# Performance work log

Measured on AMD Instinct MI355X. Metric: run time of the kernel, lower is better.

## Reference

```python
import jax, jax.numpy as jnp
import numpy as np
from jax.scipy.special import gammaln

EPS = 1e-20
EULER_GAMMA = 0.5772156649015329
B, L, D, H, DK, DV = 8, 512, 1024, 16, 64, 64
K_WEIBULL = 0.5
BETA_GAMMA = 1.0
SCALE = 1.0 / np.sqrt(DK)  # torch code DIVIDES by this -> multiply by sqrt(DK)


def setup_inputs() -> dict:
    key = jax.random.key(0)
    ks = jax.random.split(key, 20)
    f = jnp.float32
    return {
        "queries": jax.random.normal(ks[0], (B, L, D), f),
        "keys": jax.random.normal(ks[1], (B, L, D), f),
        "values": jax.random.normal(ks[2], (B, L, D), f),
        "unif": jax.random.uniform(ks[3], (B, H, L, L), f),
        "Wq": jax.random.normal(ks[4], (D, H * DK), f) * 0.03,
        "bq": jnp.zeros((H * DK,), f),
        "Wk": jax.random.normal(ks[5], (D, H * DK), f) * 0.03,
        "bk": jnp.zeros((H * DK,), f),
        "Wv": jax.random.normal(ks[6], (D, H * DV), f) * 0.03,
        "bv": jnp.zeros((H * DV,), f),
        "Wo": jax.random.normal(ks[7], (H * DV, D), f) * 0.03,
        "bo": jnp.zeros((D,), f),
        "Wp1": jax.random.normal(ks[8], (DK, D), f) * 0.05,
        "bp1": jnp.zeros((D,), f),
        "Wp2": jax.random.normal(ks[9], (D, 1), f) * 0.05,
        "bp2": jnp.zeros((1,), f),
    }


def reference(queries, keys, values, unif, Wq, bq, Wk, bk, Wv, bv, Wo, bo, Wp1, bp1, Wp2, bp2):
    # projections -> multi-head layout
    q = (queries @ Wq + bq).reshape(B, L, H, DK).transpose(0, 2, 1, 3)   # [B,H,Q,dk]
    k = (keys @ Wk + bk).reshape(B, L, H, DK).transpose(0, 2, 1, 3)     # [B,H,K,dk]
    v = (values @ Wv + bv).reshape(B, L, H, DV).transpose(0, 2, 1, 3)   # [B,H,K,dv]

    # faithful: torch divides by scale=1/sqrt(dk)
    att = jnp.einsum("bhqd,bhkd->bhqk", q, k) / SCALE                   # [B,H,Q,K]

    # prior MLP on keys (per key position)
    h = (k @ Wp1 + bp1)                                                  # [B,H,K,D]
    h = jnp.where(h >= 0, h, 0.01 * h)                                   # LeakyReLU
    dot_gamma = (h @ Wp2 + bp2).transpose(0, 1, 3, 2)                    # [B,H,1,K]
    prior_w = jax.nn.softmax(dot_gamma, axis=-1)
    alpha = prior_w * BETA_GAMMA                                         # [B,H,1,K]

    # Weibull reparameterized stochastic attention
    inv_k = 1.0 / K_WEIBULL
    logprobs = jnp.log(jax.nn.softmax(att, axis=-1) + EPS)
    gumbel_w = jnp.log(-jnp.log(1.0 - unif + EPS) + EPS)
    att_s = jax.nn.softmax(logprobs - gammaln(1.0 + inv_k + inv_k * gumbel_w), axis=-1)

    lg1 = gammaln(jnp.float32(1.0 + inv_k))
    kl = -(alpha * (logprobs - lg1)
           - EULER_GAMMA * alpha * inv_k
           - BETA_GAMMA * jnp.exp(logprobs - lg1 + lg1)
           + alpha * jnp.log(BETA_GAMMA + EPS)
           - gammaln(alpha + EPS))
    kl_mean = kl.mean()

    out = jnp.einsum("bhqk,bhkd->bhqd", att_s, v)                        # [B,H,Q,dv]
    out = out.transpose(0, 2, 1, 3).reshape(B, L, H * DV)
    out = out @ Wo + bo                                                  # [B,Q,D]
    return out, kl_mean
```

## Files before the change

### kernel.cpp

```cpp
#include <hip/hip_runtime.h>
#include <math.h>


typedef __bf16 bh_t;
typedef bh_t  bh8  __attribute__((ext_vector_type(8)));
typedef float f32x4 __attribute__((ext_vector_type(4)));
typedef _Float16 hf_t;
typedef hf_t  hf4  __attribute__((ext_vector_type(4)));

#define MFMA_BF16 __builtin_amdgcn_mfma_f32_16x16x32_bf16

static constexpr size_t P2 = 4096ull*1024ull*2ull;
static constexpr size_t W2 = 1024ull*1024ull*2ull;
static constexpr size_t O_QHI = 0;
static constexpr size_t O_QLO = O_QHI + P2;
static constexpr size_t O_KHI = O_QLO + P2;
static constexpr size_t O_KLO = O_KHI + P2;
static constexpr size_t O_VT  = O_KLO + P2;
static constexpr size_t O_WQH = O_VT  + P2;
static constexpr size_t O_WQL = O_WQH + W2;
static constexpr size_t O_WKH = O_WQL + W2;
static constexpr size_t O_WKL = O_WKH + W2;
static constexpr size_t O_WVH = O_WKL + W2;
static constexpr size_t O_WVL = O_WVH + W2;
static constexpr size_t O_WOH = O_WVL + W2;
static constexpr size_t O_WOL = O_WOH + W2;
static constexpr size_t O_WP1H = O_WOL + W2;
static constexpr size_t O_WP1L = O_WP1H + 1024ull*64ull*2ull;
static constexpr size_t O_DG   = O_WP1L + 1024ull*64ull*2ull;
static constexpr size_t O_ALPHA= O_DG + 65536ull*4ull;
static constexpr size_t O_HO   = O_ALPHA + 65536ull*4ull;
static constexpr size_t O_GS   = O_HO + P2;
static constexpr size_t O_ACC  = O_GS + 512ull*65536ull*2ull;
static constexpr size_t WS_TOTAL = O_ACC + 256;

__device__ __align__(256) unsigned char g_ws[WS_TOTAL];

__device__ __forceinline__ float lgamma_fast(float x)
{
    float ax = (x < 0.5f) ? (1.0f - x) : x;
    float p  = ax*(ax+1.f)*(ax+2.f)*(ax+3.f);
    bool  sm = ax < 4.0f;
    float lsh = sm ? __logf(p) : 0.0f;
    float y   = sm ? (ax + 4.0f) : ax;
    float ly  = __logf(y);
    float inv = __builtin_amdgcn_rcpf(y);
    float i2  = inv * inv;
    float stir = fmaf(y - 0.5f, ly, -y) + 0.91893853320467274f
               + inv * fmaf(-2.7777777777e-3f, i2, 8.3333333333e-2f);
    float core = stir - lsh;
    float r  = x - rintf(x);
    float sp = __sinf(3.14159265358979f * r);
    float rres = 1.14472988584940017f - __logf(fabsf(sp)) - core;
    return (x < 0.5f) ? rres : core;
}

__global__ void k_zero(double* a)
{
    if (threadIdx.x < 4) a[threadIdx.x] = 0.0;
}

__global__ __launch_bounds__(256) void k_transpose_split(
    const float* __restrict__ in, bh_t* __restrict__ oh, bh_t* __restrict__ ol,
    int rows, int cols)
{
    __shared__ float tile[64][65];
    const int bc = blockIdx.x * 64, br = blockIdx.y * 64;
    const int t = threadIdx.x;
    const int r = t >> 2, c0 = (t & 3) * 16;
#pragma unroll
    for (int i = 0; i < 16; i += 4) {
        float4 v = *(const float4*)(in + (size_t)(br + r) * cols + bc + c0 + i);
        tile[r][c0+i]   = v.x; tile[r][c0+i+1] = v.y;
        tile[r][c0+i+2] = v.z; tile[r][c0+i+3] = v.w;
    }
    __syncthreads();
    bh8 hv[2], lv[2];
#pragma unroll
    for (int i = 0; i < 16; i++) {
        float x = tile[c0 + i][r];
        bh_t hh = (bh_t)x;
        hv[i >> 3][i & 7] = hh;
        lv[i >> 3][i & 7] = (bh_t)(x - (float)hh);
    }
    size_t ob = (size_t)(bc + r) * rows + br + c0;
    *(bh8*)(oh + ob)     = hv[0];
    *(bh8*)(oh + ob + 8) = hv[1];
    *(bh8*)(ol + ob)     = lv[0];
    *(bh8*)(ol + ob + 8) = lv[1];
}

__global__ __launch_bounds__(256) void k_transpose_split4(
    const float* __restrict__ W0, const float* __restrict__ W1,
    const float* __restrict__ W2_, const float* __restrict__ W3,
    bh_t* __restrict__ OH)
{
    __shared__ float tile[64][65];
    const int z = blockIdx.z;
    const float* in = (z == 0) ? W0 : (z == 1) ? W1 : (z == 2) ? W2_ : W3;
    bh_t* oh = OH + (size_t)z * 2ull * 1024ull * 1024ull;
    bh_t* ol = oh + 1024ull * 1024ull;
    const int bc = blockIdx.x * 64, br = blockIdx.y * 64;
    const int t = threadIdx.x;
    const int r = t >> 2, c0 = (t & 3) * 16;
#pragma unroll
    for (int i = 0; i < 16; i += 4) {
        float4 v = *(const float4*)(in + (size_t)(br + r) * 1024 + bc + c0 + i);
        tile[r][c0+i]   = v.x; tile[r][c0+i+1] = v.y;
        tile[r][c0+i+2] = v.z; tile[r][c0+i+3] = v.w;
    }
    __syncthreads();
    bh8 hv[2], lv[2];
#pragma unroll
    for (int i = 0; i < 16; i++) {
        float x = tile[c0 + i][r];
        bh_t hh = (bh_t)x;
        hv[i >> 3][i & 7] = hh;
        lv[i >> 3][i & 7] = (bh_t)(x - (float)hh);
    }
    size_t ob = (size_t)(bc + r) * 1024 + br + c0;
    *(bh8*)(oh + ob)     = hv[0];
    *(bh8*)(oh + ob + 8) = hv[1];
    *(bh8*)(ol + ob)     = lv[0];
    *(bh8*)(ol + ob + 8) = lv[1];
}

template<bool SPLIT, int OMODE, bool ABF>
__device__ __forceinline__ void gemm_body(
    const float* __restrict__ A, const bh_t* __restrict__ ABH,
    const bh_t* __restrict__ WH, const bh_t* __restrict__ WL,
    const float* __restrict__ bias,
    bh_t* __restrict__ oh, bh_t* __restrict__ ol, float* __restrict__ of,
    int n0, int m0)
{
    __shared__ __align__(16) bh_t Ah[128][40];
    __shared__ __align__(16) bh_t Al[128][40];
    __shared__ __align__(16) bh_t Bh[64][40];
    __shared__ __align__(16) bh_t Bl[64][40];
    const int t = threadIdx.x;
    const int lane = t & 63, w = t >> 6;
    const int lr = lane & 15, kg = lane >> 4;
    const int wm = (w & 1) * 64, wn = (w >> 1) * 32;
    const int ar = t >> 2, ac = (t & 3) * 8;
    f32x4 acc[4][2] = {};

    for (int kt = 0; kt < 1024; kt += 32) {
        __syncthreads();
        {
            if constexpr (ABF) {
                *(bh8*)&Ah[ar][ac]      = *(const bh8*)(ABH + (size_t)(m0 + ar) * 1024 + kt + ac);
                *(bh8*)&Ah[ar + 64][ac] = *(const bh8*)(ABH + (size_t)(m0 + ar + 64) * 1024 + kt + ac);
            } else {
#pragma unroll
                for (int half = 0; half < 2; half++) {
                    const float* ap = A + (size_t)(m0 + ar + half*64) * 1024 + kt + ac;
                    float4 v0 = *(const float4*)ap;
                    float4 v1 = *(const float4*)(ap + 4);
                    float xs[8] = {v0.x, v0.y, v0.z, v0.w, v1.x, v1.y, v1.z, v1.w};
                    bh8 h, l;
#pragma unroll
                    for (int i = 0; i < 8; i++) {
                        bh_t hh = (bh_t)xs[i];
                        h[i] = hh;
                        l[i] = (bh_t)(xs[i] - (float)hh);
                    }
                    *(bh8*)&Ah[ar + half*64][ac] = h;
                    if constexpr (SPLIT) *(bh8*)&Al[ar + half*64][ac] = l;
                }
            }
            size_t wb = (size_t)(n0 + ar) * 1024 + kt + ac;
            *(bh8*)&Bh[ar][ac] = *(const bh8*)(WH + wb);
            if constexpr (SPLIT) *(bh8*)&Bl[ar][ac] = *(const bh8*)(WL + wb);
        }
        __syncthreads();
#pragma unroll
        for (int fm = 0; fm < 4; fm++) {
            bh8 a_h = *(bh8*)&Ah[wm + fm*16 + lr][kg * 8];
            bh8 a_l;
            if constexpr (SPLIT) a_l = *(bh8*)&Al[wm + fm*16 + lr][kg * 8];
#pragma unroll
            for (int fn = 0; fn < 2; fn++) {
                bh8 b_h = *(bh8*)&Bh[wn + fn*16 + lr][kg * 8];
                acc[fm][fn] = MFMA_BF16(a_h, b_h, acc[fm][fn], 0, 0, 0);
                if constexpr (SPLIT) {
                    bh8 b_l = *(bh8*)&Bl[wn + fn*16 + lr][kg * 8];
                    acc[fm][fn] = MFMA_BF16(a_h, b_l, acc[fm][fn], 0, 0, 0);
                    acc[fm][fn] = MFMA_BF16(a_l, b_h, acc[fm][fn], 0, 0, 0);
                }
            }
        }
    }
#pragma unroll
    for (int fm = 0; fm < 4; fm++)
#pragma unroll
    for (int fn = 0; fn < 2; fn++) {
        int col = n0 + wn + fn*16 + lr;
        float bv = bias[col];
#pragma unroll
        for (int r = 0; r < 4; r++) {
            int row = m0 + wm + fm*16 + kg*4 + r;
            float c = acc[fm][fn][r] + bv;
            size_t idx = (size_t)row * 1024 + col;
            if constexpr (OMODE == 0) {
                bh_t hh = (bh_t)c;
                oh[idx] = hh;
                ol[idx] = (bh_t)(c - (float)hh);
            } else if constexpr (OMODE == 1) {
                oh[idx] = (bh_t)c;
            } else if constexpr (OMODE == 2) {
                of[idx] = c;
            } else {
                int bb = row >> 9, ll = row & 511;
                oh[(((size_t)(bb*16 + (col >> 6)) * 64) + (col & 63)) * 512 + ll] = (bh_t)c;
            }
        }
    }
}

template<bool SPLIT, int OMODE, bool ABF>
__global__ __launch_bounds__(256) void k_gemm(
    const float* __restrict__ A, const bh_t* __restrict__ ABH,
    const bh_t* __restrict__ WH, const bh_t* __restrict__ WL,
    const float* __restrict__ bias,
    bh_t* __restrict__ oh, bh_t* __restrict__ ol, float* __restrict__ of)
{
    gemm_body<SPLIT, OMODE, ABF>(A, ABH, WH, WL, bias, oh, ol, of,
                                 blockIdx.x * 64, blockIdx.y * 128);
}

__global__ __launch_bounds__(256) void k_gemm_qk(
    const float* __restrict__ Aq, const float* __restrict__ Ak,
    const bh_t* __restrict__ Wbase, const float* __restrict__ bq,
    const float* __restrict__ bk, bh_t* __restrict__ Obase)
{
    const int z = blockIdx.z;
    const float* A = z ? Ak : Aq;
    const bh_t* WH = Wbase + (size_t)z * 2ull * 1024ull * 1024ull;
    const bh_t* WL = WH + 1024ull * 1024ull;
    const float* bias = z ? bk : bq;
    bh_t* oh = Obase + (size_t)z * 2ull * 4096ull * 1024ull;
    bh_t* ol = oh + 4096ull * 1024ull;
    gemm_body<true, 0, false>(A, nullptr, WH, WL, bias, oh, ol, nullptr,
                              blockIdx.x * 64, blockIdx.y * 128);
}

__global__ __launch_bounds__(256) void k_prior(
    const bh_t* __restrict__ KH, const bh_t* __restrict__ WP1T,
    const float* __restrict__ bp1, const float* __restrict__ wp2,
    const float* __restrict__ bp2, float* __restrict__ DG)
{
    __shared__ __align__(16) bh_t Kt[64][72];
    __shared__ __align__(16) bh_t Wt[64][72];
    const int lt = blockIdx.x, h = blockIdx.y, b = blockIdx.z;
    const int t = threadIdx.x, lane = t & 63, w = t >> 6;
    const int lr = lane & 15, kg = lane >> 4;
    {
        int r = t >> 2, j0 = (t & 3) * 16;
        const bh_t* src = KH + ((size_t)(b*512 + lt*64 + r)) * 1024 + h*64 + j0;
        *(bh8*)&Kt[r][j0]     = *(const bh8*)src;
        *(bh8*)&Kt[r][j0 + 8] = *(const bh8*)(src + 8);
    }
    __syncthreads();
    bh8 af0 = *(bh8*)&Kt[w*16 + lr][kg * 8];
    bh8 af1 = *(bh8*)&Kt[w*16 + lr][32 + kg * 8];
    float dgp[4] = {0.f, 0.f, 0.f, 0.f};
    for (int dt = 0; dt < 16; dt++) {
        __syncthreads();
        {
            int r = t >> 2, j0 = (t & 3) * 16;
            const bh_t* src = WP1T + (size_t)(dt*64 + r) * 64 + j0;
            *(bh8*)&Wt[r][j0]     = *(const bh8*)src;
            *(bh8*)&Wt[r][j0 + 8] = *(const bh8*)(src + 8);
        }
        __syncthreads();
#pragma unroll
        for (int fn = 0; fn < 4; fn++) {
            bh8 b0 = *(bh8*)&Wt[fn*16 + lr][kg * 8];
            bh8 b1 = *(bh8*)&Wt[fn*16 + lr][32 + kg * 8];
            f32x4 acc = {};
            acc = MFMA_BF16(af0, b0, acc, 0, 0, 0);
            acc = MFMA_BF16(af1, b1, acc, 0, 0, 0);
            int d = dt*64 + fn*16 + lr;
            float bpv = bp1[d], wvv = wp2[d];
#pragma unroll
            for (int r = 0; r < 4; r++) {
                float hv = acc[r] + bpv;
                hv = (hv >= 0.f) ? hv : 0.01f * hv;
                dgp[r] = fmaf(hv, wvv, dgp[r]);
            }
        }
    }
#pragma unroll
    for (int r = 0; r < 4; r++) {
        float v = dgp[r];
        v += __shfl_xor(v, 1); v += __shfl_xor(v, 2);
        v += __shfl_xor(v, 4); v += __shfl_xor(v, 8);
        dgp[r] = v;
    }
    if (lr == 0) {
        float b2 = bp2[0];
        int bh = b * 16 + h;
#pragma unroll
        for (int r = 0; r < 4; r++)
            DG[(size_t)bh*512 + lt*64 + w*16 + kg*4 + r] = dgp[r] + b2;
    }
}

__global__ __launch_bounds__(512) void k_alpha(
    const float* __restrict__ DG, float* __restrict__ AL, double* __restrict__ acc)
{
    __shared__ float red[512];
    const int bh = blockIdx.x, t = threadIdx.x;
    float v = DG[(size_t)bh * 512 + t];
    red[t] = v; __syncthreads();
    for (int s = 256; s > 0; s >>= 1) { if (t < s) red[t] = fmaxf(red[t], red[t+s]); __syncthreads(); }
    float m = red[0]; __syncthreads();
    float e = expf(v - m);
    red[t] = e; __syncthreads();
    for (int s = 256; s > 0; s >>= 1) { if (t < s) red[t] += red[t+s]; __syncthreads(); }
    float ssum = red[0]; __syncthreads();
    float a = e / ssum;
    AL[(size_t)bh * 512 + t] = a;
    float t2 = a * 1.8475785103630112f + lgammaf(a + 1e-20f);
    red[t] = t2; __syncthreads();
    for (int s = 256; s > 0; s >>= 1) { if (t < s) red[t] += red[t+s]; __syncthreads(); }
    if (t == 0) atomicAdd(&acc[2], (double)red[0]);
}

__global__ __launch_bounds__(512, 3) void k_attn(
    const bh_t* __restrict__ QH, const bh_t* __restrict__ QL,
    const bh_t* __restrict__ KH, const bh_t* __restrict__ KL,
    const bh_t* __restrict__ VT, const float* __restrict__ U,
    const float* __restrict__ AL, bh_t* __restrict__ HOB,
    hf_t* __restrict__ GS, double* __restrict__ acc)
{
    __shared__ __align__(16) bh_t KtH[64][72];
    __shared__ __align__(16) bh_t KtL[64][72];
    __shared__ __align__(16) bh_t Vt[64][72];
    __shared__ __align__(16) bh_t Sl[8][16][72];
    __shared__ float Asm[64];
    __shared__ float red[512];

    const int flat = blockIdx.x;
    const int bh = flat & 127, qc = flat >> 7;
    const int b = bh >> 4, h = bh & 15;
    const int t = threadIdx.x, w = t >> 6, lane = t & 63;
    const int lr = lane & 15, kg = lane >> 4;
    const int q0 = qc * 128 + w * 16;
    const int sr = t >> 3, sj = (t & 7) * 8;
    const float* Up = U + ((size_t)bh * 512 + q0 + kg * 4) * 512;
    hf_t* GSp = GS + (size_t)flat * 65536 + (size_t)w * 8192;

    bh8 qh[2], ql[2];
    {
        size_t qb = ((size_t)(b * 512) + q0 + lr) * 1024 + h * 64;
        qh[0] = *(const bh8*)(QH + qb + kg * 8);
        qh[1] = *(const bh8*)(QH + qb + 32 + kg * 8);
        ql[0] = *(const bh8*)(QL + qb + kg * 8);
        ql[1] = *(const bh8*)(QL + qb + 32 + kg * 8);
    }
    float C[4];

    {
        float M1[4], Z1[4];
#pragma unroll
        for (int r = 0; r < 4; r++) { M1[r] = -INFINITY; Z1[r] = 0.f; }

        for (int kt = 0; kt < 8; kt++) {
            __syncthreads();
            {
                size_t src = ((size_t)(b*512 + kt*64 + sr)) * 1024 + h*64 + sj;
                *(bh8*)&KtH[sr][sj] = *(const bh8*)(KH + src);
                *(bh8*)&KtL[sr][sj] = *(const bh8*)(KL + src);
            }
            __syncthreads();
            f32x4 av[4];
#pragma unroll
            for (int fn = 0; fn < 4; fn++) {
                f32x4 a = {};
#pragma unroll
                for (int ks = 0; ks < 2; ks++) {
                    bh8 kb  = *(bh8*)&KtH[fn*16 + lr][ks*32 + kg*8];
                    bh8 kl2 = *(bh8*)&KtL[fn*16 + lr][ks*32 + kg*8];
                    a = MFMA_BF16(qh[ks], kb,  a, 0, 0, 0);
                    a = MFMA_BF16(qh[ks], kl2, a, 0, 0, 0);
                    a = MFMA_BF16(ql[ks], kb,  a, 0, 0, 0);
                }
#pragma unroll
                for (int r = 0; r < 4; r++) a[r] *= 8.0f;
                av[fn] = a;
                int k = kt * 64 + fn * 16 + lr;
                hf4 gh;
#pragma unroll
                for (int r = 0; r < 4; r++) {
                    float u  = Up[(size_t)r * 512 + k];
                    float tt = (1.0f - u) + 1e-20f;
                    float gl = 1e-20f - __logf(tt);
                    float g  = __logf(gl);
                    gh[r] = (hf_t)lgamma_fast(fmaf(2.0f, g, 3.0f));
                }
                *(hf4*)(GSp + ((size_t)(kt*4 + fn) * 64 + lane) * 4) = gh;
            }
#pragma unroll
            for (int r = 0; r < 4; r++) {
                float mx = fmaxf(fmaxf(av[0][r], av[1][r]), fmaxf(av[2][r], av[3][r]));
                mx = fmaxf(mx, __shfl_xor(mx, 1));
                mx = fmaxf(mx, __shfl_xor(mx, 2));
                mx = fmaxf(mx, __shfl_xor(mx, 4));
                mx = fmaxf(mx, __shfl_xor(mx, 8));
                float nm = fmaxf(M1[r], mx);
                float es = __expf(av[0][r]-nm) + __expf(av[1][r]-nm)
                         + __expf(av[2][r]-nm) + __expf(av[3][r]-nm);
                es += __shfl_xor(es, 1); es += __shfl_xor(es, 2);
                es += __shfl_xor(es, 4); es += __shfl_xor(es, 8);
                Z1[r] = Z1[r] * __expf(M1[r] - nm) + es;
                M1[r] = nm;
            }
        }
#pragma unroll
        for (int r = 0; r < 4; r++) C[r] = M1[r] + logf(Z1[r]);
    }

    float M2[4], Z2[4];
    f32x4 oacc[4] = {};
#pragma unroll
    for (int r = 0; r < 4; r++) { M2[r] = -INFINITY; Z2[r] = 0.f; }
    float S1f = 0.f;

    for (int kt = 0; kt < 8; kt++) {
        __syncthreads();
        {
            size_t src = ((size_t)(b*512 + kt*64 + sr)) * 1024 + h*64 + sj;
            *(bh8*)&KtH[sr][sj] = *(const bh8*)(KH + src);
            *(bh8*)&KtL[sr][sj] = *(const bh8*)(KL + src);
            const bh_t* vsrc = VT + ((size_t)bh * 64 + sr) * 512 + kt*64 + sj;
            *(bh8*)&Vt[sr][sj] = *(const bh8*)vsrc;
            if (t < 64) Asm[t] = AL[(size_t)bh * 512 + kt * 64 + t];
        }
        __syncthreads();
        f32x4 wv[4];
#pragma unroll
        for (int fn = 0; fn < 4; fn++) {
            f32x4 a = {};
#pragma unroll
            for (int ks = 0; ks < 2; ks++) {
                bh8 kb  = *(bh8*)&KtH[fn*16 + lr][ks*32 + kg*8];
                bh8 kl2 = *(bh8*)&KtL[fn*16 + lr][ks*32 + kg*8];
                a = MFMA_BF16(qh[ks], kb,  a, 0, 0, 0);
                a = MFMA_BF16(qh[ks], kl2, a, 0, 0, 0);
                a = MFMA_BF16(ql[ks], kb,  a, 0, 0, 0);
            }
            hf4 gh = *(const hf4*)(GSp + ((size_t)(kt*4 + fn) * 64 + lane) * 4);
            float alv = Asm[fn * 16 + lr];
#pragma unroll
            for (int r = 0; r < 4; r++) {
                float s  = fmaf(a[r], 8.0f, -C[r]);
                float ex = __expf(s);
                float lp = __logf(ex + 1e-20f);
                wv[fn][r] = lp - (float)gh[r];
                S1f = fmaf(alv, lp, S1f);
            }
        }
#pragma unroll
        for (int r = 0; r < 4; r++) {
            float mx = fmaxf(fmaxf(wv[0][r], wv[1][r]), fmaxf(wv[2][r], wv[3][r]));
            mx = fmaxf(mx, __shfl_xor(mx, 1));
            mx = fmaxf(mx, __shfl_xor(mx, 2));
            mx = fmaxf(mx, __shfl_xor(mx, 4));
            mx = fmaxf(mx, __shfl_xor(mx, 8));
            float nm = fmaxf(M2[r], mx);
            float sc = __expf(M2[r] - nm);
            float zs = 0.f;
#pragma unroll
            for (int fn = 0; fn < 4; fn++) {
                float sv = __expf(wv[fn][r] - nm);
                zs += sv;
                Sl[w][kg * 4 + r][fn * 16 + lr] = (bh_t)sv;
            }
            zs += __shfl_xor(zs, 1); zs += __shfl_xor(zs, 2);
            zs += __shfl_xor(zs, 4); zs += __shfl_xor(zs, 8);
            Z2[r] = fmaf(Z2[r], sc, zs);
            M2[r] = nm;
#pragma unroll
            for (int fo = 0; fo < 4; fo++) oacc[fo][r] *= sc;
        }
        bh8 sa0 = *(bh8*)&Sl[w][lr][kg*8];
        bh8 sa1 = *(bh8*)&Sl[w][lr][32 + kg*8];
#pragma unroll
        for (int fo = 0; fo < 4; fo++) {
            bh8 v0 = *(bh8*)&Vt[fo*16 + lr][kg*8];
            bh8 v1 = *(bh8*)&Vt[fo*16 + lr][32 + kg*8];
            oacc[fo] = MFMA_BF16(sa0, v0, oacc[fo], 0, 0, 0);
            oacc[fo] = MFMA_BF16(sa1, v1, oacc[fo], 0, 0, 0);
        }
    }
    float rz[4];
#pragma unroll
    for (int r = 0; r < 4; r++) rz[r] = 1.0f / Z2[r];
#pragma unroll
    for (int fo = 0; fo < 4; fo++) {
#pragma unroll
        for (int r = 0; r < 4; r++) {
            int q = q0 + kg * 4 + r;
            int dv = fo * 16 + lr;
            HOB[((size_t)(b * 512 + q)) * 1024 + h * 64 + dv] = (bh_t)(oacc[fo][r] * rz[r]);
        }
    }
    red[t] = S1f; __syncthreads();
    for (int s = 256; s > 0; s >>= 1) { if (t < s) red[t] += red[t+s]; __syncthreads(); }
    if (t == 0) atomicAdd(&acc[0], (double)red[0]);
}

__global__ void k_kl(const double* __restrict__ acc, float* __restrict__ out)
{
    if (threadIdx.x == 0 && blockIdx.x == 0) {
        double kl = (-acc[0] + 512.0 * acc[2] + 65536.0) / 33554432.0;
        out[4194304] = (float)kl;
    }
}

extern "C" void kernel_launch(void* const* d_in, const int* in_sizes, int n_in,
                              void* d_out, int out_size, void* d_ws, size_t ws_size,
                              hipStream_t stream)
{
    (void)in_sizes; (void)n_in; (void)d_ws; (void)ws_size; (void)out_size;
    const float* queries = (const float*)d_in[0];
    const float* keys    = (const float*)d_in[1];
    const float* values  = (const float*)d_in[2];
    const float* unif    = (const float*)d_in[3];
    const float* Wq = (const float*)d_in[4];  const float* bq = (const float*)d_in[5];
    const float* Wk = (const float*)d_in[6];  const float* bk = (const float*)d_in[7];
    const float* Wv = (const float*)d_in[8];  const float* bv = (const float*)d_in[9];
    const float* Wo = (const float*)d_in[10]; const float* bo = (const float*)d_in[11];
    const float* Wp1 = (const float*)d_in[12]; const float* bp1 = (const float*)d_in[13];
    const float* Wp2 = (const float*)d_in[14]; const float* bp2 = (const float*)d_in[15];

    unsigned char* ws = nullptr;
    hipGetSymbolAddress((void**)&ws, HIP_SYMBOL(g_ws));

    bh_t* QHI = (bh_t*)(ws + O_QHI);
    bh_t* KHI = (bh_t*)(ws + O_KHI); bh_t* KLO = (bh_t*)(ws + O_KLO);
    bh_t* QLO = (bh_t*)(ws + O_QLO);
    bh_t* VTp = (bh_t*)(ws + O_VT);
    bh_t* WQH = (bh_t*)(ws + O_WQH);
    bh_t* WVH = (bh_t*)(ws + O_WVH); bh_t* WVL = (bh_t*)(ws + O_WVL);
    bh_t* WOH = (bh_t*)(ws + O_WOH); bh_t* WOL = (bh_t*)(ws + O_WOL);
    bh_t* WP1H = (bh_t*)(ws + O_WP1H); bh_t* WP1L = (bh_t*)(ws + O_WP1L);
    float* DG    = (float*)(ws + O_DG);
    float* ALPHA = (float*)(ws + O_ALPHA);
    bh_t*  HOB   = (bh_t*)(ws + O_HO);
    hf_t*  GS    = (hf_t*)(ws + O_GS);
    double* ACC  = (double*)(ws + O_ACC);
    float* outF  = (float*)d_out;

    k_zero<<<1, 64, 0, stream>>>(ACC);

    k_transpose_split4<<<dim3(16,16,4), 256, 0, stream>>>(Wq, Wk, Wv, Wo, WQH);
    k_transpose_split<<<dim3(16,1), 256, 0, stream>>>(Wp1, WP1H, WP1L, 64, 1024);

    k_gemm_qk<<<dim3(16,32,2), 256, 0, stream>>>(queries, keys, WQH, bq, bk, QHI);
    k_gemm<false,3,false><<<dim3(16,32), 256, 0, stream>>>(values, nullptr, WVH, WVL, bv, VTp, nullptr, nullptr);

    k_prior<<<dim3(8,16,8), 256, 0, stream>>>(KHI, WP1H, bp1, Wp2, bp2, DG);
    k_alpha<<<128, 512, 0, stream>>>(DG, ALPHA, ACC);

    k_attn<<<512, 512, 0, stream>>>(QHI, QLO, KHI, KLO, VTp, unif, ALPHA, HOB, GS, ACC);

    k_gemm<false,2,true><<<dim3(16,32), 256, 0, stream>>>(nullptr, HOB, WOH, WOL, bo, nullptr, nullptr, outF);
    k_kl<<<1, 1, 0, stream>>>(ACC, outF);
}
```

Baseline: 358.8 us.

## Pre-split activations to bf16, enlarge GEMM tile to 128x128, fuse tiny kernels

Adds a separate kernel that converts the query, key and value activations to bf16 hi/lo pairs once, so the GEMM blocks no longer repeat the fp32 conversion on every tile load. The GEMM tile grows from 128x64 to 128x128 with B fragments hoisted into registers, which gives more MFMA reuse per loaded element and halves the number of blocks. The accumulator zeroing and the final KL write are folded into existing kernels, removing two launches. In exchange it adds extra workspace traffic for the split activations, uses more registers and LDS per block, and launches fewer blocks, which may underfill the GPU.

```diff
diff --git a/kernel.cpp b/kernel.cpp
--- a/kernel.cpp
+++ b/kernel.cpp
@@ -10,7 +10,8 @@
 
 #define MFMA_BF16 __builtin_amdgcn_mfma_f32_16x16x32_bf16
 
-static constexpr size_t P2 = 4096ull*1024ull*2ull;
+static constexpr size_t PE = 4096ull*1024ull;
+static constexpr size_t P2 = PE*2ull;
 static constexpr size_t W2 = 1024ull*1024ull*2ull;
 static constexpr size_t O_QHI = 0;
 static constexpr size_t O_QLO = O_QHI + P2;
@@ -32,7 +33,8 @@
 static constexpr size_t O_HO   = O_ALPHA + 65536ull*4ull;
 static constexpr size_t O_GS   = O_HO + P2;
 static constexpr size_t O_ACC  = O_GS + 512ull*65536ull*2ull;
-static constexpr size_t WS_TOTAL = O_ACC + 256;
+static constexpr size_t O_AQH  = O_ACC + 256;
+static constexpr size_t WS_TOTAL = O_AQH + 5ull*P2;
 
 __device__ __align__(256) unsigned char g_ws[WS_TOTAL];
 
@@ -55,11 +57,6 @@
     return (x < 0.5f) ? rres : core;
 }
 
-__global__ void k_zero(double* a)
-{
-    if (threadIdx.x < 4) a[threadIdx.x] = 0.0;
-}
-
 __global__ __launch_bounds__(256) void k_transpose_split(
     const float* __restrict__ in, bh_t* __restrict__ oh, bh_t* __restrict__ ol,
     int rows, int cols)
@@ -93,10 +90,12 @@
 __global__ __launch_bounds__(256) void k_transpose_split4(
     const float* __restrict__ W0, const float* __restrict__ W1,
     const float* __restrict__ W2_, const float* __restrict__ W3,
-    bh_t* __restrict__ OH)
+    bh_t* __restrict__ OH, double* __restrict__ acc)
 {
     __shared__ float tile[64][65];
     const int z = blockIdx.z;
+    if (z == 0 && blockIdx.x == 0 && blockIdx.y == 0 && threadIdx.x < 4)
+        acc[threadIdx.x] = 0.0;
     const float* in = (z == 0) ? W0 : (z == 1) ? W1 : (z == 2) ? W2_ : W3;
     bh_t* oh = OH + (size_t)z * 2ull * 1024ull * 1024ull;
     bh_t* ol = oh + 1024ull * 1024ull;
@@ -125,9 +124,35 @@
     *(bh8*)(ol + ob + 8) = lv[1];
 }
 
-template<bool SPLIT, int OMODE, bool ABF>
+__global__ __launch_bounds__(256) void k_splitA(
+    const float* __restrict__ q, const float* __restrict__ k,
+    const float* __restrict__ v, bh_t* __restrict__ dst)
+{
+    const int z = blockIdx.y;
+    const float* in = (z == 0) ? q : (z == 1) ? k : v;
+    size_t idx = ((size_t)blockIdx.x * 256 + threadIdx.x) * 8;
+    float4 v0 = *(const float4*)(in + idx);
+    float4 v1 = *(const float4*)(in + idx + 4);
+    float xs[8] = {v0.x, v0.y, v0.z, v0.w, v1.x, v1.y, v1.z, v1.w};
+    bh8 h, l;
+#pragma unroll
+    for (int i = 0; i < 8; i++) {
+        bh_t hh = (bh_t)xs[i];
+        h[i] = hh;
+        l[i] = (bh_t)(xs[i] - (float)hh);
+    }
+    if (z < 2) {
+        bh_t* hp = dst + (size_t)z * 2 * PE;
+        *(bh8*)(hp + idx)      = h;
+        *(bh8*)(hp + PE + idx) = l;
+    } else {
+        *(bh8*)(dst + 4 * PE + idx) = h;
+    }
+}
+
+template<bool SPLIT, int OMODE>
 __device__ __forceinline__ void gemm_body(
-    const float* __restrict__ A, const bh_t* __restrict__ ABH,
+    const bh_t* __restrict__ ABH, const bh_t* __restrict__ ABL,
     const bh_t* __restrict__ WH, const bh_t* __restrict__ WL,
     const float* __restrict__ bias,
     bh_t* __restrict__ oh, bh_t* __restrict__ ol, float* __restrict__ of,
@@ -135,57 +160,53 @@
 {
     __shared__ __align__(16) bh_t Ah[128][40];
     __shared__ __align__(16) bh_t Al[128][40];
-    __shared__ __align__(16) bh_t Bh[64][40];
-    __shared__ __align__(16) bh_t Bl[64][40];
+    __shared__ __align__(16) bh_t Bh[128][40];
+    __shared__ __align__(16) bh_t Bl[128][40];
     const int t = threadIdx.x;
     const int lane = t & 63, w = t >> 6;
     const int lr = lane & 15, kg = lane >> 4;
-    const int wm = (w & 1) * 64, wn = (w >> 1) * 32;
+    const int wm = (w & 1) * 64, wn = (w >> 1) * 64;
     const int ar = t >> 2, ac = (t & 3) * 8;
-    f32x4 acc[4][2] = {};
+    f32x4 acc[4][4] = {};
 
     for (int kt = 0; kt < 1024; kt += 32) {
         __syncthreads();
         {
-            if constexpr (ABF) {
-                *(bh8*)&Ah[ar][ac]      = *(const bh8*)(ABH + (size_t)(m0 + ar) * 1024 + kt + ac);
-                *(bh8*)&Ah[ar + 64][ac] = *(const bh8*)(ABH + (size_t)(m0 + ar + 64) * 1024 + kt + ac);
-            } else {
-#pragma unroll
-                for (int half = 0; half < 2; half++) {
-                    const float* ap = A + (size_t)(m0 + ar + half*64) * 1024 + kt + ac;
-                    float4 v0 = *(const float4*)ap;
-                    float4 v1 = *(const float4*)(ap + 4);
-                    float xs[8] = {v0.x, v0.y, v0.z, v0.w, v1.x, v1.y, v1.z, v1.w};
-                    bh8 h, l;
-#pragma unroll
-                    for (int i = 0; i < 8; i++) {
-                        bh_t hh = (bh_t)xs[i];
-                        h[i] = hh;
-                        l[i] = (bh_t)(xs[i] - (float)hh);
-                    }
-                    *(bh8*)&Ah[ar + half*64][ac] = h;
-                    if constexpr (SPLIT) *(bh8*)&Al[ar + half*64][ac] = l;
-                }
-            }
-            size_t wb = (size_t)(n0 + ar) * 1024 + kt + ac;
-            *(bh8*)&Bh[ar][ac] = *(const bh8*)(WH + wb);
-            if constexpr (SPLIT) *(bh8*)&Bl[ar][ac] = *(const bh8*)(WL + wb);
+            size_t a0 = (size_t)(m0 + ar) * 1024 + kt + ac;
+            size_t a1 = (size_t)(m0 + ar + 64) * 1024 + kt + ac;
+            *(bh8*)&Ah[ar][ac]      = *(const bh8*)(ABH + a0);
+            *(bh8*)&Ah[ar + 64][ac] = *(const bh8*)(ABH + a1);
+            if constexpr (SPLIT) {
+                *(bh8*)&Al[ar][ac]      = *(const bh8*)(ABL + a0);
+                *(bh8*)&Al[ar + 64][ac] = *(const bh8*)(ABL + a1);
+            }
+            size_t b0 = (size_t)(n0 + ar) * 1024 + kt + ac;
+            size_t b1 = (size_t)(n0 + ar + 64) * 1024 + kt + ac;
+            *(bh8*)&Bh[ar][ac]      = *(const bh8*)(WH + b0);
+            *(bh8*)&Bh[ar + 64][ac] = *(const bh8*)(WH + b1);
+            if constexpr (SPLIT) {
+                *(bh8*)&Bl[ar][ac]      = *(const bh8*)(WL + b0);
+                *(bh8*)&Bl[ar + 64][ac] = *(const bh8*)(WL + b1);
+            }
         }
         __syncthreads();
+        bh8 bfh[4], bfl[4];
+#pragma unroll
+        for (int fn = 0; fn < 4; fn++) {
+            bfh[fn] = *(bh8*)&Bh[wn + fn*16 + lr][kg * 8];
+            if constexpr (SPLIT) bfl[fn] = *(bh8*)&Bl[wn + fn*16 + lr][kg * 8];
+        }
 #pragma unroll
         for (int fm = 0; fm < 4; fm++) {
             bh8 a_h = *(bh8*)&Ah[wm + fm*16 + lr][kg * 8];
             bh8 a_l;
             if constexpr (SPLIT) a_l = *(bh8*)&Al[wm + fm*16 + lr][kg * 8];
 #pragma unroll
-            for (int fn = 0; fn < 2; fn++) {
-                bh8 b_h = *(bh8*)&Bh[wn + fn*16 + lr][kg * 8];
-                acc[fm][fn] = MFMA_BF16(a_h, b_h, acc[fm][fn], 0, 0, 0);
+            for (int fn = 0; fn < 4; fn++) {
+                acc[fm][fn] = MFMA_BF16(a_h, bfh[fn], acc[fm][fn], 0, 0, 0);
                 if constexpr (SPLIT) {
-                    bh8 b_l = *(bh8*)&Bl[wn + fn*16 + lr][kg * 8];
-                    acc[fm][fn] = MFMA_BF16(a_h, b_l, acc[fm][fn], 0, 0, 0);
-                    acc[fm][fn] = MFMA_BF16(a_l, b_h, acc[fm][fn], 0, 0, 0);
+                    acc[fm][fn] = MFMA_BF16(a_h, bfl[fn], acc[fm][fn], 0, 0, 0);
+                    acc[fm][fn] = MFMA_BF16(a_l, bfh[fn], acc[fm][fn], 0, 0, 0);
                 }
             }
         }
@@ -193,7 +214,7 @@
 #pragma unroll
     for (int fm = 0; fm < 4; fm++)
 #pragma unroll
-    for (int fn = 0; fn < 2; fn++) {
+    for (int fn = 0; fn < 4; fn++) {
         int col = n0 + wn + fn*16 + lr;
         float bv = bias[col];
 #pragma unroll
@@ -217,31 +238,36 @@
     }
 }
 
-template<bool SPLIT, int OMODE, bool ABF>
+template<int OMODE>
 __global__ __launch_bounds__(256) void k_gemm(
-    const float* __restrict__ A, const bh_t* __restrict__ ABH,
+    const bh_t* __restrict__ ABH,
     const bh_t* __restrict__ WH, const bh_t* __restrict__ WL,
     const float* __restrict__ bias,
-    bh_t* __restrict__ oh, bh_t* __restrict__ ol, float* __restrict__ of)
-{
-    gemm_body<SPLIT, OMODE, ABF>(A, ABH, WH, WL, bias, oh, ol, of,
-                                 blockIdx.x * 64, blockIdx.y * 128);
+    bh_t* __restrict__ oh, float* __restrict__ of,
+    const double* __restrict__ acc)
+{
+    gemm_body<false, OMODE>(ABH, nullptr, WH, WL, bias, oh, nullptr, of,
+                            blockIdx.x * 128, blockIdx.y * 128);
+    if constexpr (OMODE == 2) {
+        if (blockIdx.x == 0 && blockIdx.y == 0 && threadIdx.x == 0) {
+            double kl = (-acc[0] + 512.0 * acc[2] + 65536.0) / 33554432.0;
+            of[4194304] = (float)kl;
+        }
+    }
 }
 
 __global__ __launch_bounds__(256) void k_gemm_qk(
-    const float* __restrict__ Aq, const float* __restrict__ Ak,
-    const bh_t* __restrict__ Wbase, const float* __restrict__ bq,
-    const float* __restrict__ bk, bh_t* __restrict__ Obase)
+    const bh_t* __restrict__ Abase, const bh_t* __restrict__ Wbase,
+    const float* __restrict__ bq, const float* __restrict__ bk,
+    bh_t* __restrict__ Obase)
 {
     const int z = blockIdx.z;
-    const float* A = z ? Ak : Aq;
+    const bh_t* AH = Abase + (size_t)z * 2 * PE;
     const bh_t* WH = Wbase + (size_t)z * 2ull * 1024ull * 1024ull;
-    const bh_t* WL = WH + 1024ull * 1024ull;
-    const float* bias = z ? bk : bq;
-    bh_t* oh = Obase + (size_t)z * 2ull * 4096ull * 1024ull;
-    bh_t* ol = oh + 4096ull * 1024ull;
-    gemm_body<true, 0, false>(A, nullptr, WH, WL, bias, oh, ol, nullptr,
-                              blockIdx.x * 64, blockIdx.y * 128);
+    bh_t* oh = Obase + (size_t)z * 2 * PE;
+    gemm_body<true, 0>(AH, AH + PE, WH, WH + 1024ull*1024ull,
+                       z ? bk : bq, oh, oh + PE, nullptr,
+                       blockIdx.x * 128, blockIdx.y * 128);
 }
 
 __global__ __launch_bounds__(256) void k_prior(
@@ -511,14 +537,6 @@
     if (t == 0) atomicAdd(&acc[0], (double)red[0]);
 }
 
-__global__ void k_kl(const double* __restrict__ acc, float* __restrict__ out)
-{
-    if (threadIdx.x == 0 && blockIdx.x == 0) {
-        double kl = (-acc[0] + 512.0 * acc[2] + 65536.0) / 33554432.0;
-        out[4194304] = (float)kl;
-    }
-}
-
 extern "C" void kernel_launch(void* const* d_in, const int* in_sizes, int n_in,
                               void* d_out, int out_size, void* d_ws, size_t ws_size,
                               hipStream_t stream)
@@ -538,9 +556,8 @@
     unsigned char* ws = nullptr;
     hipGetSymbolAddress((void**)&ws, HIP_SYMBOL(g_ws));
 
-    bh_t* QHI = (bh_t*)(ws + O_QHI);
+    bh_t* QHI = (bh_t*)(ws + O_QHI); bh_t* QLO = (bh_t*)(ws + O_QLO);
     bh_t* KHI = (bh_t*)(ws + O_KHI); bh_t* KLO = (bh_t*)(ws + O_KLO);
-    bh_t* QLO = (bh_t*)(ws + O_QLO);
     bh_t* VTp = (bh_t*)(ws + O_VT);
     bh_t* WQH = (bh_t*)(ws + O_WQH);
     bh_t* WVH = (bh_t*)(ws + O_WVH); bh_t* WVL = (bh_t*)(ws + O_WVL);
@@ -551,21 +568,21 @@
     bh_t*  HOB   = (bh_t*)(ws + O_HO);
     hf_t*  GS    = (hf_t*)(ws + O_GS);
     double* ACC  = (double*)(ws + O_ACC);
+    bh_t*  AQH   = (bh_t*)(ws + O_AQH);
+    bh_t*  AVH   = AQH + 4 * PE;
     float* outF  = (float*)d_out;
 
-    k_zero<<<1, 64, 0, stream>>>(ACC);
-
-    k_transpose_split4<<<dim3(16,16,4), 256, 0, stream>>>(Wq, Wk, Wv, Wo, WQH);
+    k_transpose_split4<<<dim3(16,16,4), 256, 0, stream>>>(Wq, Wk, Wv, Wo, WQH, ACC);
     k_transpose_split<<<dim3(16,1), 256, 0, stream>>>(Wp1, WP1H, WP1L, 64, 1024);
-
-    k_gemm_qk<<<dim3(16,32,2), 256, 0, stream>>>(queries, keys, WQH, bq, bk, QHI);
-    k_gemm<false,3,false><<<dim3(16,32), 256, 0, stream>>>(values, nullptr, WVH, WVL, bv, VTp, nullptr, nullptr);
+    k_splitA<<<dim3(2048,3), 256, 0, stream>>>(queries, keys, values, AQH);
+
+    k_gemm_qk<<<dim3(8,32,2), 256, 0, stream>>>(AQH, WQH, bq, bk, QHI);
+    k_gemm<3><<<dim3(8,32), 256, 0, stream>>>(AVH, WVH, WVL, bv, VTp, nullptr, nullptr);
 
     k_prior<<<dim3(8,16,8), 256, 0, stream>>>(KHI, WP1H, bp1, Wp2, bp2, DG);
     k_alpha<<<128, 512, 0, stream>>>(DG, ALPHA, ACC);
 
     k_attn<<<512, 512, 0, stream>>>(QHI, QLO, KHI, KLO, VTp, unif, ALPHA, HOB, GS, ACC);
 
-    k_gemm<false,2,true><<<dim3(16,32), 256, 0, stream>>>(nullptr, HOB, WOH, WOL, bo, nullptr, nullptr, outF);
-    k_kl<<<1, 1, 0, stream>>>(ACC, outF);
-}
+    k_gemm<2><<<dim3(8,32), 256, 0, stream>>>(HOB, WOH, WOL, bo, nullptr, outF, ACC);
+}
```

Result: faster. 339.7 us (-5.3%).
